# Optimization experiments

Measured on AMD Instinct MI355X. Metric: run time of the kernel, lower is better.

Reference implementation:

```python
import jax, jax.numpy as jnp
import numpy as np

N_NODES = 20000
N_EDGES = 640000
D = 128          # vision_dim == topo_dim
OUT = 256        # out_dim
B = 64           # image batch == num graphs
HW = 64
NEG_SLOPE = 0.2


def _sn(w2d, u):
    """PyTorch spectral_norm forward: one power iteration (u,v detached), W/sigma."""
    v = jax.lax.stop_gradient(w2d.T @ u)
    v = v / (jnp.linalg.norm(v) + 1e-12)
    u2 = jax.lax.stop_gradient(w2d @ v)
    u2 = u2 / (jnp.linalg.norm(u2) + 1e-12)
    sigma = u2 @ (w2d @ v)
    return w2d / sigma


def _leaky(x):
    return jnp.where(x >= 0, x, NEG_SLOPE * x)


def setup_inputs() -> dict:
    key = jax.random.key(0)
    ks = jax.random.split(key, 16)
    vis = jax.random.normal(ks[0], (B, D, HW, HW), dtype=jnp.float32)
    topo = jax.random.normal(ks[1], (N_NODES, D), dtype=jnp.float32)
    edge_index = jax.random.randint(ks[2], (2, N_EDGES), 0, N_NODES, dtype=jnp.int64)
    batch = jnp.sort(jax.random.randint(ks[3], (N_NODES,), 0, B, dtype=jnp.int64))
    s = 0.05
    conv_w = jax.random.normal(ks[4], (D, D, 3, 3), dtype=jnp.float32) * s
    conv_b = jnp.zeros((D,), dtype=jnp.float32)
    conv_u = jax.random.normal(ks[5], (D,), dtype=jnp.float32)
    fcv_w = jax.random.normal(ks[6], (OUT, D * 4), dtype=jnp.float32) * s
    fcv_b = jnp.zeros((OUT,), dtype=jnp.float32)
    fcv_u = jax.random.normal(ks[7], (OUT,), dtype=jnp.float32)
    gcn_w = jax.random.normal(ks[8], (D, D), dtype=jnp.float32) * s
    gcn_b = jnp.zeros((D,), dtype=jnp.float32)
    fct_w = jax.random.normal(ks[9], (OUT, D), dtype=jnp.float32) * s
    fct_b = jnp.zeros((OUT,), dtype=jnp.float32)
    fct_u = jax.random.normal(ks[10], (OUT,), dtype=jnp.float32)
    return dict(vis=vis, topo=topo, edge_index=edge_index, batch=batch,
                conv_w=conv_w, conv_b=conv_b, conv_u=conv_u,
                fcv_w=fcv_w, fcv_b=fcv_b, fcv_u=fcv_u,
                gcn_w=gcn_w, gcn_b=gcn_b,
                fct_w=fct_w, fct_b=fct_b, fct_u=fct_u)


def reference(vis, topo, edge_index, batch,
              conv_w, conv_b, conv_u,
              fcv_w, fcv_b, fcv_u,
              gcn_w, gcn_b,
              fct_w, fct_b, fct_u):
    # ---- vision head: spectral-norm conv3x3 -> leaky_relu -> adaptive max pool 2x2 -> SN linear
    cw = _sn(conv_w.reshape(D, -1), conv_u).reshape(conv_w.shape)
    x = jax.lax.conv_general_dilated(vis, cw, window_strides=(1, 1), padding='VALID',
                                     dimension_numbers=('NCHW', 'OIHW', 'NCHW'))
    x = _leaky(x + conv_b[None, :, None, None])              # [B, D, 62, 62]
    Bc, C, H, W = x.shape
    x = x.reshape(Bc, C, 2, H // 2, 2, W // 2).max(axis=(3, 5))  # adaptive max pool -> [B,D,2,2]
    x = x.reshape(Bc, -1)                                    # [B, 4D]
    vis_score = x @ _sn(fcv_w, fcv_u).T + fcv_b              # [B, OUT]

    # ---- topo head: GCNConv (sym-norm, self-loops) -> leaky_relu -> global max pool -> SN linear
    n = topo.shape[0]
    loop = jnp.arange(n, dtype=edge_index.dtype)
    src = jnp.concatenate([edge_index[0], loop])
    dst = jnp.concatenate([edge_index[1], loop])
    deg = jax.ops.segment_sum(jnp.ones_like(dst, dtype=topo.dtype), dst, num_segments=n)
    dis = jnp.where(deg > 0, jax.lax.rsqrt(jnp.maximum(deg, 1.0)), 0.0)
    norm = dis[src] * dis[dst]                               # [E+N]
    xw = topo @ gcn_w                                        # [N, D]
    h = jax.ops.segment_sum(norm[:, None] * xw[src], dst, num_segments=n) + gcn_b
    h = _leaky(h)
    pooled = jax.ops.segment_max(h, batch, num_segments=B)   # [B, D]
    topo_score = pooled @ _sn(fct_w, fct_u).T + fct_b        # [B, OUT]

    return (vis_score, topo_score)
```

## Files before the change

### kernel.cpp

```cpp
#include <hip/hip_runtime.h>
#include <hip/hip_bf16.h>
#include <float.h>
#include <stdint.h>

#define NB   64
#define CD   128
#define OUTD 256
#define NNODE 20000
#define NEDGE 640000

typedef __bf16 bf16x8 __attribute__((ext_vector_type(8)));
typedef float  f32x4  __attribute__((ext_vector_type(4)));

__device__ inline void gl_lds16(const void* g, void* l) {
  __builtin_amdgcn_global_load_lds(
      (const __attribute__((address_space(1))) void*)g,
      (__attribute__((address_space(3))) void*)l, 16, 0, 0);
}

__device__ inline void atomicMaxF(float* addr, float val) {
  if (val >= 0.f) atomicMax((int*)addr, __float_as_int(val));
  else            atomicMin((unsigned int*)addr, __float_as_uint(val));
}

__global__ void k_init(float* __restrict__ pooled_v, float* __restrict__ pooled_t,
                       int* __restrict__ cnt, int* __restrict__ fill,
                       float* __restrict__ sn_scratch, int* __restrict__ ntotal) {
  const int i = blockIdx.x * 256 + threadIdx.x;
  if (i < NB * CD * 4) pooled_v[i] = -FLT_MAX;
  if (i < NB * CD)     pooled_t[i] = -FLT_MAX;
  if (i < NNODE)       { cnt[i] = 0; fill[i] = 0; }
  if (i < 1796)        sn_scratch[i] = 0.0f;
  if (i == 0)          *ntotal = 0;
}

__global__ __launch_bounds__(256) void k_sn_v(const float* __restrict__ conv_w, const float* __restrict__ conv_u,
                                              const float* __restrict__ fcv_w,  const float* __restrict__ fcv_u,
                                              const float* __restrict__ fct_w,  const float* __restrict__ fct_u,
                                              float* __restrict__ sn) {
  const int bb = blockIdx.x;
  const float* W; const float* u; float* v; int C; int r0;
  if (bb < 4)       { W = conv_w; u = conv_u; v = sn;        C = 1152; r0 = bb * 32; }
  else if (bb < 12) { W = fcv_w;  u = fcv_u;  v = sn + 1152; C = 512;  r0 = (bb - 4) * 32; }
  else              { W = fct_w;  u = fct_u;  v = sn + 1664; C = 128;  r0 = (bb - 12) * 32; }
  const int tid = threadIdx.x;
  float acc[5] = {0.f, 0.f, 0.f, 0.f, 0.f};
  for (int i = r0; i < r0 + 32; ++i) {
    const float ui = u[i];
    const float* row = W + (size_t)i * C;
    #pragma unroll
    for (int t = 0; t < 5; ++t) {
      const int j = tid + t * 256;
      if (j < C) acc[t] += ui * row[j];
    }
  }
  #pragma unroll
  for (int t = 0; t < 5; ++t) {
    const int j = tid + t * 256;
    if (j < C) atomicAdd(&v[j], acc[t]);
  }
}

__global__ __launch_bounds__(256) void k_sn_w(const float* __restrict__ conv_w,
                                              const float* __restrict__ fcv_w,
                                              const float* __restrict__ fct_w,
                                              float* __restrict__ sn) {
  const int gw = blockIdx.x * 4 + (threadIdx.x >> 6);
  const int lane = threadIdx.x & 63;
  const float* W; const float* v; int C, m, row;
  if (gw < 128)      { W = conv_w; v = sn;        C = 1152; m = 0; row = gw; }
  else if (gw < 384) { W = fcv_w;  v = sn + 1152; C = 512;  m = 1; row = gw - 128; }
  else               { W = fct_w;  v = sn + 1664; C = 128;  m = 2; row = gw - 384; }
  const float* wr = W + (size_t)row * C;
  float y = 0.f;
  for (int c = lane; c < C; c += 64) y += wr[c] * v[c];
  #pragma unroll
  for (int s = 32; s > 0; s >>= 1) y += __shfl_xor(y, s, 64);
  if (lane == 0) atomicAdd(&sn[1792 + m], y * y);
}

__global__ __launch_bounds__(256) void k_sn_fin(const float* __restrict__ sn, float* __restrict__ inv_sigma) {
  __shared__ float red[256];
  const int tid = threadIdx.x;
  const int off[4] = {0, 1152, 1664, 1792};
  for (int m = 0; m < 3; ++m) {
    const int C = off[m + 1] - off[m];
    float ss = 0.f;
    for (int j = tid; j < C; j += 256) { const float a = sn[off[m] + j]; ss += a * a; }
    red[tid] = ss; __syncthreads();
    for (int s = 128; s > 0; s >>= 1) { if (tid < s) red[tid] += red[tid + s]; __syncthreads(); }
    if (tid == 0) inv_sigma[m] = (sqrtf(red[0]) + 1e-12f) / sqrtf(sn[1792 + m]);
    __syncthreads();
  }
}

__global__ void k_pack(const float* __restrict__ conv_w, const float* __restrict__ inv_sigma,
                       __hip_bfloat16* __restrict__ Bt2) {
  const int t = blockIdx.x * 256 + threadIdx.x;
  if (t >= 147456) return;
  const int j = t & 7, n = (t >> 3) & 127, s = (t >> 10) & 7, hk = (t >> 13) & 1, tap = t >> 14;
  const int ci = hk * 64 + s * 8 + j;
  Bt2[t] = __float2bfloat16(conv_w[n * 1152 + ci * 9 + tap] * inv_sigma[0]);
}

__global__ __launch_bounds__(256) void k_transpose(const float* __restrict__ vis,
                                                   __hip_bfloat16* __restrict__ visT2) {
  __shared__ float tile[8192];
  const int by = blockIdx.x;
  const int b = by >> 6, y = by & 63;
  const int t = threadIdx.x;
  const float* src = vis + (size_t)b * 524288 + (size_t)(t >> 6) * 4096 + y * 64 + (t & 63);
  #pragma unroll
  for (int i = 0; i < 32; ++i)
    tile[(i * 4 + (t >> 6)) * 64 + (t & 63)] = src[(size_t)i * 4 * 4096];
  __syncthreads();
  bf16x8* dst = (bf16x8*)(visT2 + ((size_t)by << 13));
  #pragma unroll
  for (int k = 0; k < 4; ++k) {
    const int j = k * 256 + t;
    const int g = j >> 6, x = j & 63;
    union { bf16x8 v; __hip_bfloat16 h[8]; } u;
    #pragma unroll
    for (int cc = 0; cc < 8; ++cc)
      u.h[cc] = __float2bfloat16(tile[(g * 8 + cc) * 64 + x]);
    dst[j] = u.v;
  }
}

__global__ __launch_bounds__(256, 4) void k_conv(const __hip_bfloat16* __restrict__ visT2,
                                                 const __hip_bfloat16* __restrict__ Bt2,
                                                 const float* __restrict__ conv_b,
                                                 float* __restrict__ pooled_v) {
  __shared__ bf16x8 lds_a[1024];
  __shared__ bf16x8 lds_b[1024];
  const int bx = blockIdx.x;
  const int b = bx / 31;
  const int y0 = (bx - b * 31) * 2;
  const int tid = threadIdx.x;
  const int wave = tid >> 6, lane = tid & 63;
  const int quad = lane >> 4, l15 = lane & 15;

  f32x4 acc[8][2];
  #pragma unroll
  for (int i = 0; i < 8; ++i) {
    acc[i][0] = f32x4{0.f, 0.f, 0.f, 0.f};
    acc[i][1] = f32x4{0.f, 0.f, 0.f, 0.f};
  }

  const __hip_bfloat16* vb = visT2 + ((size_t)b << 19);
  const int s0 = wave << 1;
  bf16x8* ldsA0 = &lds_a[s0 << 7];
  bf16x8* ldsB0 = &lds_b[s0 << 7];
  const int lane8 = lane << 3;

  for (int ky = 0; ky < 3; ++ky) {
    for (int kx = 0; kx < 3; ++kx) {
      const int tap = ky * 3 + kx;
      #pragma unroll
      for (int hk = 0; hk < 2; ++hk) {
        const __hip_bfloat16* a0p = vb + ((size_t)(((y0 + ky) << 4) + (hk << 3) + s0) << 9) + (kx << 3) + lane8;
        const __hip_bfloat16* a1p = vb + ((size_t)(((y0 + 1 + ky) << 4) + (hk << 3) + s0) << 9) + (kx << 3) + lane8;
        const __hip_bfloat16* bp  = Bt2 + (((size_t)(((tap << 1) + hk) << 3) + s0) << 10) + lane8;
        gl_lds16(a0p,        ldsA0);
        gl_lds16(a1p,        ldsA0 + 64);
        gl_lds16(a0p + 512,  ldsA0 + 128);
        gl_lds16(a1p + 512,  ldsA0 + 192);
        gl_lds16(bp,         ldsB0);
        gl_lds16(bp + 512,   ldsB0 + 64);
        gl_lds16(bp + 1024,  ldsB0 + 128);
        gl_lds16(bp + 1536,  ldsB0 + 192);
        __syncthreads();
        const bf16x8 b00 = lds_b[(quad << 7) + (wave << 5) + l15];
        const bf16x8 b01 = lds_b[(quad << 7) + (wave << 5) + 16 + l15];
        const bf16x8 b10 = lds_b[((4 + quad) << 7) + (wave << 5) + l15];
        const bf16x8 b11 = lds_b[((4 + quad) << 7) + (wave << 5) + 16 + l15];
        #pragma unroll
        for (int mt = 0; mt < 8; ++mt) {
          const bf16x8 a0 = lds_a[(quad << 7) + (mt << 4) + l15];
          const bf16x8 a1 = lds_a[((4 + quad) << 7) + (mt << 4) + l15];
          acc[mt][0] = __builtin_amdgcn_mfma_f32_16x16x32_bf16(a0, b00, acc[mt][0], 0, 0, 0);
          acc[mt][1] = __builtin_amdgcn_mfma_f32_16x16x32_bf16(a0, b01, acc[mt][1], 0, 0, 0);
          acc[mt][0] = __builtin_amdgcn_mfma_f32_16x16x32_bf16(a1, b10, acc[mt][0], 0, 0, 0);
          acc[mt][1] = __builtin_amdgcn_mfma_f32_16x16x32_bf16(a1, b11, acc[mt][1], 0, 0, 0);
        }
        __syncthreads();
      }
    }
  }

  const float cb0 = conv_b[(wave << 5) + l15];
  const float cb1 = conv_b[(wave << 5) + 16 + l15];
  float pmax[2][2][2];
  #pragma unroll
  for (int i = 0; i < 8; ++i) (&pmax[0][0][0])[i] = -FLT_MAX;

  #pragma unroll
  for (int mt = 0; mt < 8; ++mt) {
    const int py = (y0 + (mt >> 2)) >= 31 ? 1 : 0;
    #pragma unroll
    for (int r = 0; r < 4; ++r) {
      const int x = ((mt & 3) << 4) + (quad << 2) + r;
      if (x < 62) {
        const int px = x >= 31 ? 1 : 0;
        float v0 = acc[mt][0][r] + cb0;  v0 = v0 >= 0.f ? v0 : 0.2f * v0;
        float v1 = acc[mt][1][r] + cb1;  v1 = v1 >= 0.f ? v1 : 0.2f * v1;
        pmax[0][py][px] = fmaxf(pmax[0][py][px], v0);
        pmax[1][py][px] = fmaxf(pmax[1][py][px], v1);
      }
    }
  }
  #pragma unroll
  for (int nt = 0; nt < 2; ++nt)
    #pragma unroll
    for (int py = 0; py < 2; ++py)
      #pragma unroll
      for (int px = 0; px < 2; ++px) {
        float v = pmax[nt][py][px];
        v = fmaxf(v, __shfl_xor(v, 16, 64));
        v = fmaxf(v, __shfl_xor(v, 32, 64));
        if (quad == 0) {
          const int n = (wave << 5) + (nt << 4) + l15;
          atomicMaxF(&pooled_v[(size_t)b * 512 + n * 4 + py * 2 + px], v);
        }
      }
}

__global__ __launch_bounds__(256) void k_fcv(const float* __restrict__ pooled_v, const float* __restrict__ fcv_w,
                                             const float* __restrict__ fcv_b, const float* __restrict__ inv_sigma,
                                             float* __restrict__ out) {
  __shared__ f32x4 xr[128];
  const int b = blockIdx.x, tid = threadIdx.x;
  if (tid < 128) xr[tid] = ((const f32x4*)pooled_v)[b * 128 + tid];
  __syncthreads();
  const f32x4* wr = (const f32x4*)(fcv_w + (size_t)tid * 512);
  f32x4 a4 = {0.f, 0.f, 0.f, 0.f};
  for (int f = 0; f < 128; ++f) {
    const f32x4 x = xr[f];
    const f32x4 w = wr[f];
    #pragma unroll
    for (int k = 0; k < 4; ++k) a4[k] += x[k] * w[k];
  }
  const float a = a4[0] + a4[1] + a4[2] + a4[3];
  out[b * 256 + tid] = a * inv_sigma[1] + fcv_b[tid];
}

__global__ void k_deg(const int* __restrict__ dst, int* __restrict__ cnt) {
  const int e = blockIdx.x * 256 + threadIdx.x;
  if (e < NEDGE) atomicAdd(&cnt[dst[e]], 1);
}

__global__ __launch_bounds__(256) void k_scan(const int* __restrict__ cnt, int* __restrict__ offset,
                                              int* __restrict__ total) {
  __shared__ int red[256];
  __shared__ int sbase;
  const int tid = threadIdx.x;
  const int n = blockIdx.x * 256 + tid;
  const int v = (n < NNODE) ? cnt[n] : 0;
  red[tid] = v; __syncthreads();
  for (int d = 1; d < 256; d <<= 1) {
    const int t = (tid >= d) ? red[tid - d] : 0;
    __syncthreads();
    red[tid] += t;
    __syncthreads();
  }
  if (tid == 255) sbase = atomicAdd(total, red[255]);
  __syncthreads();
  if (n < NNODE) offset[n] = sbase + red[tid] - v;
}

__global__ void k_bucket(const int* __restrict__ src, const int* __restrict__ dst,
                         const int* __restrict__ offset, int* __restrict__ fill,
                         int* __restrict__ sorted_src) {
  const int e = blockIdx.x * 256 + threadIdx.x;
  if (e >= NEDGE) return;
  const int t = dst[e];
  const int pos = atomicAdd(&fill[t], 1);
  sorted_src[offset[t] + pos] = src[e];
}

__global__ void k_dis(const int* __restrict__ cnt, float* __restrict__ dis) {
  const int n = blockIdx.x * 256 + threadIdx.x;
  if (n < NNODE) dis[n] = rsqrtf((float)(cnt[n] + 1));
}

__global__ __launch_bounds__(256) void k_xw(const float* __restrict__ topo, const float* __restrict__ gcn_w,
                                            float* __restrict__ xw) {
  __shared__ f32x4 w4[4096];
  const int tid = threadIdx.x;
  const f32x4* gw4 = (const f32x4*)gcn_w;
  for (int i = tid; i < 4096; i += 256) w4[i] = gw4[i];
  __syncthreads();
  const int n0 = blockIdx.x * 64;
  const int jq = tid & 31, ns = tid >> 5;
  for (int pass = 0; pass < 8; ++pass) {
    const int n = n0 + pass * 8 + ns;
    if (n >= NNODE) break;
    const f32x4* tr4 = (const f32x4*)(topo + (size_t)n * 128);
    f32x4 a = {0.f, 0.f, 0.f, 0.f};
    for (int d4 = 0; d4 < 32; ++d4) {
      const f32x4 t = tr4[d4];
      const int base = (d4 << 7) + jq;
      #pragma unroll
      for (int m = 0; m < 4; ++m) {
        const f32x4 w = w4[base + m * 32];
        #pragma unroll
        for (int k = 0; k < 4; ++k) a[k] += t[m] * w[k];
      }
    }
    ((f32x4*)xw)[(size_t)n * 32 + jq] = a;
  }
}

__global__ __launch_bounds__(256) void k_gather(const int* __restrict__ sorted_src,
                                                const int* __restrict__ offset, const int* __restrict__ cnt,
                                                const float* __restrict__ dis, const float* __restrict__ xw,
                                                const float* __restrict__ gcn_b, float* __restrict__ h) {
  __shared__ f32x4 red[256];
  const int n = blockIdx.x;
  const int tid = threadIdx.x;
  const int es = tid >> 5;
  const int d4 = tid & 31;
  const int e0 = offset[n], ne = cnt[n];
  const float dn = dis[n];
  const f32x4* xw4 = (const f32x4*)xw;
  f32x4 a = {0.f, 0.f, 0.f, 0.f};
  if (es == 0) {
    const f32x4 x = xw4[(size_t)n * 32 + d4];
    #pragma unroll
    for (int k = 0; k < 4; ++k) a[k] = dn * x[k];
  }
  for (int e = es; e < ne; e += 8) {
    const int s = sorted_src[e0 + e];
    const float w = dis[s];
    const f32x4 x = xw4[(size_t)s * 32 + d4];
    #pragma unroll
    for (int k = 0; k < 4; ++k) a[k] += w * x[k];
  }
  red[tid] = a;
  __syncthreads();
  if (tid < 128) {
    #pragma unroll
    for (int k = 0; k < 4; ++k) red[tid][k] += red[tid + 128][k];
  }
  __syncthreads();
  if (tid < 64) {
    #pragma unroll
    for (int k = 0; k < 4; ++k) red[tid][k] += red[tid + 64][k];
  }
  __syncthreads();
  if (tid < 32) {
    f32x4 r = red[tid];
    const f32x4 r2 = red[tid + 32];
    const f32x4 gb = ((const f32x4*)gcn_b)[tid];
    f32x4 v;
    #pragma unroll
    for (int k = 0; k < 4; ++k) {
      float t = gb[k] + dn * (r[k] + r2[k]);
      v[k] = t >= 0.f ? t : 0.2f * t;
    }
    ((f32x4*)h)[(size_t)n * 32 + tid] = v;
  }
}

__global__ void k_pool_t(const float* __restrict__ h, const int* __restrict__ batch,
                         float* __restrict__ pooled_t) {
  const int d = threadIdx.x;
  const int n0 = blockIdx.x * 32;
  float run = -FLT_MAX;
  int cur = batch[n0];
  for (int i = 0; i < 32; ++i) {
    const int n = n0 + i;
    const int g = batch[n];
    if (g != cur) {
      atomicMaxF(&pooled_t[cur * 128 + d], run);
      run = -FLT_MAX; cur = g;
    }
    run = fmaxf(run, h[(size_t)n * 128 + d]);
  }
  atomicMaxF(&pooled_t[cur * 128 + d], run);
}

__global__ __launch_bounds__(256) void k_fct(const float* __restrict__ pooled_t, const float* __restrict__ fct_w,
                                             const float* __restrict__ fct_b, const float* __restrict__ inv_sigma,
                                             float* __restrict__ out) {
  __shared__ f32x4 xr[32];
  const int b = blockIdx.x, tid = threadIdx.x;
  if (tid < 32) xr[tid] = ((const f32x4*)pooled_t)[b * 32 + tid];
  __syncthreads();
  const f32x4* wr = (const f32x4*)(fct_w + (size_t)tid * 128);
  f32x4 a4 = {0.f, 0.f, 0.f, 0.f};
  for (int f = 0; f < 32; ++f) {
    const f32x4 x = xr[f];
    const f32x4 w = wr[f];
    #pragma unroll
    for (int k = 0; k < 4; ++k) a4[k] += x[k] * w[k];
  }
  const float a = a4[0] + a4[1] + a4[2] + a4[3];
  out[NB * 256 + b * 256 + tid] = a * inv_sigma[2] + fct_b[tid];
}

extern "C" void kernel_launch(void* const* d_in, const int* in_sizes, int n_in,
                              void* d_out, int out_size, void* d_ws, size_t ws_size,
                              hipStream_t stream) {
  const float* vis    = (const float*)d_in[0];
  const float* topo   = (const float*)d_in[1];
  const int*   eidx   = (const int*)d_in[2];
  const int*   batch  = (const int*)d_in[3];
  const float* conv_w = (const float*)d_in[4];
  const float* conv_b = (const float*)d_in[5];
  const float* conv_u = (const float*)d_in[6];
  const float* fcv_w  = (const float*)d_in[7];
  const float* fcv_b  = (const float*)d_in[8];
  const float* fcv_u  = (const float*)d_in[9];
  const float* gcn_w  = (const float*)d_in[10];
  const float* gcn_b  = (const float*)d_in[11];
  const float* fct_w  = (const float*)d_in[12];
  const float* fct_b  = (const float*)d_in[13];
  const float* fct_u  = (const float*)d_in[14];
  float* out = (float*)d_out;

  char* p = (char*)d_ws;
  float* inv_sigma  = (float*)p; p += 256;
  float* sn_scratch = (float*)p; p += 1796 * 4 + 240;
  float* pooled_v   = (float*)p; p += (size_t)NB * 512 * 4;
  float* pooled_t   = (float*)p; p += (size_t)NB * 128 * 4;
  int*   cnt        = (int*)p;   p += (size_t)NNODE * 4;
  int*   offset     = (int*)p;   p += (size_t)NNODE * 4;
  int*   fill       = (int*)p;   p += (size_t)NNODE * 4;
  float* dis        = (float*)p; p += (size_t)NNODE * 4;
  int*   ntotal     = (int*)p;   p += 256;
  int*   sorted_src = (int*)p;   p += (size_t)NEDGE * 4;
  float* xw         = (float*)p; p += (size_t)NNODE * 128 * 4;
  float* h          = (float*)p; p += (size_t)NNODE * 128 * 4;
  __hip_bfloat16* Bt2 = (__hip_bfloat16*)p; p += (size_t)147456 * 2;
  p = (char*)(((uintptr_t)p + 255) & ~(uintptr_t)255);
  __hip_bfloat16* visT2 = (__hip_bfloat16*)p;

  hipLaunchKernelGGL(k_init,      dim3(128),   dim3(256), 0, stream, pooled_v, pooled_t, cnt, fill, sn_scratch, ntotal);
  hipLaunchKernelGGL(k_sn_v,      dim3(20),    dim3(256), 0, stream, conv_w, conv_u, fcv_w, fcv_u, fct_w, fct_u, sn_scratch);
  hipLaunchKernelGGL(k_sn_w,      dim3(160),   dim3(256), 0, stream, conv_w, fcv_w, fct_w, sn_scratch);
  hipLaunchKernelGGL(k_sn_fin,    dim3(1),     dim3(256), 0, stream, sn_scratch, inv_sigma);
  hipLaunchKernelGGL(k_pack,      dim3(576),   dim3(256), 0, stream, conv_w, inv_sigma, Bt2);
  hipLaunchKernelGGL(k_transpose, dim3(4096),  dim3(256), 0, stream, vis, visT2);
  hipLaunchKernelGGL(k_conv,      dim3(64*31), dim3(256), 0, stream, visT2, Bt2, conv_b, pooled_v);
  hipLaunchKernelGGL(k_fcv,       dim3(64),    dim3(256), 0, stream, pooled_v, fcv_w, fcv_b, inv_sigma, out);
  hipLaunchKernelGGL(k_deg,       dim3(2500),  dim3(256), 0, stream, eidx + NEDGE, cnt);
  hipLaunchKernelGGL(k_scan,      dim3(79),    dim3(256), 0, stream, cnt, offset, ntotal);
  hipLaunchKernelGGL(k_bucket,    dim3(2500),  dim3(256), 0, stream, eidx, eidx + NEDGE, offset, fill, sorted_src);
  hipLaunchKernelGGL(k_dis,       dim3(79),    dim3(256), 0, stream, cnt, dis);
  hipLaunchKernelGGL(k_xw,        dim3(313),   dim3(256), 0, stream, topo, gcn_w, xw);
  hipLaunchKernelGGL(k_gather,    dim3(NNODE), dim3(256), 0, stream, sorted_src, offset, cnt, dis, xw, gcn_b, h);
  hipLaunchKernelGGL(k_pool_t,    dim3(625),   dim3(128), 0, stream, h, batch, pooled_t);
  hipLaunchKernelGGL(k_fct,       dim3(64),    dim3(256), 0, stream, pooled_t, fct_w, fct_b, inv_sigma, out);
}
```

Measured before the change: 588.2 us.

## Store prescaled xw and h in bf16, wave-per-node gather, fuse small kernels

```diff
diff --git a/kernel.cpp b/kernel.cpp
--- a/kernel.cpp
+++ b/kernel.cpp
@@ -10,6 +10,7 @@
 #define NEDGE 640000
 
 typedef __bf16 bf16x8 __attribute__((ext_vector_type(8)));
+typedef __bf16 bf16x4 __attribute__((ext_vector_type(4)));
 typedef float  f32x4  __attribute__((ext_vector_type(4)));
 
 __device__ inline void gl_lds16(const void* g, void* l) {
@@ -225,32 +226,13 @@
       }
 }
 
-__global__ __launch_bounds__(256) void k_fcv(const float* __restrict__ pooled_v, const float* __restrict__ fcv_w,
-                                             const float* __restrict__ fcv_b, const float* __restrict__ inv_sigma,
-                                             float* __restrict__ out) {
-  __shared__ f32x4 xr[128];
-  const int b = blockIdx.x, tid = threadIdx.x;
-  if (tid < 128) xr[tid] = ((const f32x4*)pooled_v)[b * 128 + tid];
-  __syncthreads();
-  const f32x4* wr = (const f32x4*)(fcv_w + (size_t)tid * 512);
-  f32x4 a4 = {0.f, 0.f, 0.f, 0.f};
-  for (int f = 0; f < 128; ++f) {
-    const f32x4 x = xr[f];
-    const f32x4 w = wr[f];
-    #pragma unroll
-    for (int k = 0; k < 4; ++k) a4[k] += x[k] * w[k];
-  }
-  const float a = a4[0] + a4[1] + a4[2] + a4[3];
-  out[b * 256 + tid] = a * inv_sigma[1] + fcv_b[tid];
-}
-
 __global__ void k_deg(const int* __restrict__ dst, int* __restrict__ cnt) {
   const int e = blockIdx.x * 256 + threadIdx.x;
   if (e < NEDGE) atomicAdd(&cnt[dst[e]], 1);
 }
 
 __global__ __launch_bounds__(256) void k_scan(const int* __restrict__ cnt, int* __restrict__ offset,
-                                              int* __restrict__ total) {
+                                              int* __restrict__ total, float* __restrict__ dis) {
   __shared__ int red[256];
   __shared__ int sbase;
   const int tid = threadIdx.x;
@@ -265,7 +247,10 @@
   }
   if (tid == 255) sbase = atomicAdd(total, red[255]);
   __syncthreads();
-  if (n < NNODE) offset[n] = sbase + red[tid] - v;
+  if (n < NNODE) {
+    offset[n] = sbase + red[tid] - v;
+    dis[n] = rsqrtf((float)(v + 1));
+  }
 }
 
 __global__ void k_bucket(const int* __restrict__ src, const int* __restrict__ dst,
@@ -278,13 +263,8 @@
   sorted_src[offset[t] + pos] = src[e];
 }
 
-__global__ void k_dis(const int* __restrict__ cnt, float* __restrict__ dis) {
-  const int n = blockIdx.x * 256 + threadIdx.x;
-  if (n < NNODE) dis[n] = rsqrtf((float)(cnt[n] + 1));
-}
-
 __global__ __launch_bounds__(256) void k_xw(const float* __restrict__ topo, const float* __restrict__ gcn_w,
-                                            float* __restrict__ xw) {
+                                            const float* __restrict__ dis, __bf16* __restrict__ xws) {
   __shared__ f32x4 w4[4096];
   const int tid = threadIdx.x;
   const f32x4* gw4 = (const f32x4*)gcn_w;
@@ -307,62 +287,57 @@
         for (int k = 0; k < 4; ++k) a[k] += t[m] * w[k];
       }
     }
-    ((f32x4*)xw)[(size_t)n * 32 + jq] = a;
+    const float dn = dis[n];
+    bf16x4 o;
+    #pragma unroll
+    for (int k = 0; k < 4; ++k) o[k] = (__bf16)(a[k] * dn);
+    ((bf16x4*)xws)[(size_t)n * 32 + jq] = o;
   }
 }
 
 __global__ __launch_bounds__(256) void k_gather(const int* __restrict__ sorted_src,
                                                 const int* __restrict__ offset, const int* __restrict__ cnt,
-                                                const float* __restrict__ dis, const float* __restrict__ xw,
-                                                const float* __restrict__ gcn_b, float* __restrict__ h) {
-  __shared__ f32x4 red[256];
-  const int n = blockIdx.x;
-  const int tid = threadIdx.x;
-  const int es = tid >> 5;
-  const int d4 = tid & 31;
+                                                const float* __restrict__ dis, const __bf16* __restrict__ xws,
+                                                const float* __restrict__ gcn_b, __bf16* __restrict__ h) {
+  const int wave = threadIdx.x >> 6, lane = threadIdx.x & 63;
+  const int n = blockIdx.x * 4 + wave;
+  const int slot = lane >> 4, l16 = lane & 15;
   const int e0 = offset[n], ne = cnt[n];
-  const float dn = dis[n];
-  const f32x4* xw4 = (const f32x4*)xw;
-  f32x4 a = {0.f, 0.f, 0.f, 0.f};
-  if (es == 0) {
-    const f32x4 x = xw4[(size_t)n * 32 + d4];
-    #pragma unroll
-    for (int k = 0; k < 4; ++k) a[k] = dn * x[k];
-  }
-  for (int e = es; e < ne; e += 8) {
+  const bf16x8* x8 = (const bf16x8*)xws;
+  float a[8];
+  if (slot == 0) {
+    const bf16x8 v = x8[(size_t)n * 16 + l16];
+    #pragma unroll
+    for (int k = 0; k < 8; ++k) a[k] = (float)v[k];
+  } else {
+    #pragma unroll
+    for (int k = 0; k < 8; ++k) a[k] = 0.f;
+  }
+  for (int e = slot; e < ne; e += 4) {
     const int s = sorted_src[e0 + e];
-    const float w = dis[s];
-    const f32x4 x = xw4[(size_t)s * 32 + d4];
-    #pragma unroll
-    for (int k = 0; k < 4; ++k) a[k] += w * x[k];
-  }
-  red[tid] = a;
-  __syncthreads();
-  if (tid < 128) {
-    #pragma unroll
-    for (int k = 0; k < 4; ++k) red[tid][k] += red[tid + 128][k];
-  }
-  __syncthreads();
-  if (tid < 64) {
-    #pragma unroll
-    for (int k = 0; k < 4; ++k) red[tid][k] += red[tid + 64][k];
-  }
-  __syncthreads();
-  if (tid < 32) {
-    f32x4 r = red[tid];
-    const f32x4 r2 = red[tid + 32];
-    const f32x4 gb = ((const f32x4*)gcn_b)[tid];
-    f32x4 v;
-    #pragma unroll
-    for (int k = 0; k < 4; ++k) {
-      float t = gb[k] + dn * (r[k] + r2[k]);
-      v[k] = t >= 0.f ? t : 0.2f * t;
-    }
-    ((f32x4*)h)[(size_t)n * 32 + tid] = v;
-  }
-}
-
-__global__ void k_pool_t(const float* __restrict__ h, const int* __restrict__ batch,
+    const bf16x8 v = x8[(size_t)s * 16 + l16];
+    #pragma unroll
+    for (int k = 0; k < 8; ++k) a[k] += (float)v[k];
+  }
+  #pragma unroll
+  for (int k = 0; k < 8; ++k) {
+    a[k] += __shfl_xor(a[k], 16, 64);
+    a[k] += __shfl_xor(a[k], 32, 64);
+  }
+  if (slot == 0) {
+    const float dn = dis[n];
+    bf16x8 o;
+    #pragma unroll
+    for (int k = 0; k < 8; ++k) {
+      float t = gcn_b[(l16 << 3) + k] + dn * a[k];
+      t = t >= 0.f ? t : 0.2f * t;
+      o[k] = (__bf16)t;
+    }
+    ((bf16x8*)h)[(size_t)n * 16 + l16] = o;
+  }
+}
+
+__global__ void k_pool_t(const __bf16* __restrict__ h, const int* __restrict__ batch,
                          float* __restrict__ pooled_t) {
   const int d = threadIdx.x;
   const int n0 = blockIdx.x * 32;
@@ -375,28 +350,48 @@
       atomicMaxF(&pooled_t[cur * 128 + d], run);
       run = -FLT_MAX; cur = g;
     }
-    run = fmaxf(run, h[(size_t)n * 128 + d]);
+    run = fmaxf(run, (float)h[(size_t)n * 128 + d]);
   }
   atomicMaxF(&pooled_t[cur * 128 + d], run);
 }
 
-__global__ __launch_bounds__(256) void k_fct(const float* __restrict__ pooled_t, const float* __restrict__ fct_w,
-                                             const float* __restrict__ fct_b, const float* __restrict__ inv_sigma,
-                                             float* __restrict__ out) {
-  __shared__ f32x4 xr[32];
-  const int b = blockIdx.x, tid = threadIdx.x;
-  if (tid < 32) xr[tid] = ((const f32x4*)pooled_t)[b * 32 + tid];
-  __syncthreads();
-  const f32x4* wr = (const f32x4*)(fct_w + (size_t)tid * 128);
-  f32x4 a4 = {0.f, 0.f, 0.f, 0.f};
-  for (int f = 0; f < 32; ++f) {
-    const f32x4 x = xr[f];
-    const f32x4 w = wr[f];
-    #pragma unroll
-    for (int k = 0; k < 4; ++k) a4[k] += x[k] * w[k];
-  }
-  const float a = a4[0] + a4[1] + a4[2] + a4[3];
-  out[NB * 256 + b * 256 + tid] = a * inv_sigma[2] + fct_b[tid];
+__global__ __launch_bounds__(256) void k_fc(const float* __restrict__ pooled_v, const float* __restrict__ fcv_w,
+                                            const float* __restrict__ fcv_b,
+                                            const float* __restrict__ pooled_t, const float* __restrict__ fct_w,
+                                            const float* __restrict__ fct_b,
+                                            const float* __restrict__ inv_sigma, float* __restrict__ out) {
+  const int tid = threadIdx.x;
+  if (blockIdx.x < 64) {
+    __shared__ f32x4 xr[128];
+    const int b = blockIdx.x;
+    if (tid < 128) xr[tid] = ((const f32x4*)pooled_v)[b * 128 + tid];
+    __syncthreads();
+    const f32x4* wr = (const f32x4*)(fcv_w + (size_t)tid * 512);
+    f32x4 a4 = {0.f, 0.f, 0.f, 0.f};
+    for (int f = 0; f < 128; ++f) {
+      const f32x4 x = xr[f];
+      const f32x4 w = wr[f];
+      #pragma unroll
+      for (int k = 0; k < 4; ++k) a4[k] += x[k] * w[k];
+    }
+    const float a = a4[0] + a4[1] + a4[2] + a4[3];
+    out[b * 256 + tid] = a * inv_sigma[1] + fcv_b[tid];
+  } else {
+    __shared__ f32x4 xr2[32];
+    const int b = blockIdx.x - 64;
+    if (tid < 32) xr2[tid] = ((const f32x4*)pooled_t)[b * 32 + tid];
+    __syncthreads();
+    const f32x4* wr = (const f32x4*)(fct_w + (size_t)tid * 128);
+    f32x4 a4 = {0.f, 0.f, 0.f, 0.f};
+    for (int f = 0; f < 32; ++f) {
+      const f32x4 x = xr2[f];
+      const f32x4 w = wr[f];
+      #pragma unroll
+      for (int k = 0; k < 4; ++k) a4[k] += x[k] * w[k];
+    }
+    const float a = a4[0] + a4[1] + a4[2] + a4[3];
+    out[NB * 256 + b * 256 + tid] = a * inv_sigma[2] + fct_b[tid];
+  }
 }
 
 extern "C" void kernel_launch(void* const* d_in, const int* in_sizes, int n_in,
@@ -430,8 +425,8 @@
   float* dis        = (float*)p; p += (size_t)NNODE * 4;
   int*   ntotal     = (int*)p;   p += 256;
   int*   sorted_src = (int*)p;   p += (size_t)NEDGE * 4;
-  float* xw         = (float*)p; p += (size_t)NNODE * 128 * 4;
-  float* h          = (float*)p; p += (size_t)NNODE * 128 * 4;
+  __bf16* xws       = (__bf16*)p; p += (size_t)NNODE * 128 * 2 + 256;
+  __bf16* h         = (__bf16*)p; p += (size_t)NNODE * 128 * 2 + 256;
   __hip_bfloat16* Bt2 = (__hip_bfloat16*)p; p += (size_t)147456 * 2;
   p = (char*)(((uintptr_t)p + 255) & ~(uintptr_t)255);
   __hip_bfloat16* visT2 = (__hip_bfloat16*)p;
@@ -443,13 +438,11 @@
   hipLaunchKernelGGL(k_pack,      dim3(576),   dim3(256), 0, stream, conv_w, inv_sigma, Bt2);
   hipLaunchKernelGGL(k_transpose, dim3(4096),  dim3(256), 0, stream, vis, visT2);
   hipLaunchKernelGGL(k_conv,      dim3(64*31), dim3(256), 0, stream, visT2, Bt2, conv_b, pooled_v);
-  hipLaunchKernelGGL(k_fcv,       dim3(64),    dim3(256), 0, stream, pooled_v, fcv_w, fcv_b, inv_sigma, out);
   hipLaunchKernelGGL(k_deg,       dim3(2500),  dim3(256), 0, stream, eidx + NEDGE, cnt);
-  hipLaunchKernelGGL(k_scan,      dim3(79),    dim3(256), 0, stream, cnt, offset, ntotal);
+  hipLaunchKernelGGL(k_scan,      dim3(79),    dim3(256), 0, stream, cnt, offset, ntotal, dis);
   hipLaunchKernelGGL(k_bucket,    dim3(2500),  dim3(256), 0, stream, eidx, eidx + NEDGE, offset, fill, sorted_src);
-  hipLaunchKernelGGL(k_dis,       dim3(79),    dim3(256), 0, stream, cnt, dis);
-  hipLaunchKernelGGL(k_xw,        dim3(313),   dim3(256), 0, stream, topo, gcn_w, xw);
-  hipLaunchKernelGGL(k_gather,    dim3(NNODE), dim3(256), 0, stream, sorted_src, offset, cnt, dis, xw, gcn_b, h);
+  hipLaunchKernelGGL(k_xw,        dim3(313),   dim3(256), 0, stream, topo, gcn_w, dis, xws);
+  hipLaunchKernelGGL(k_gather,    dim3(5000),  dim3(256), 0, stream, sorted_src, offset, cnt, dis, xws, gcn_b, h);
   hipLaunchKernelGGL(k_pool_t,    dim3(625),   dim3(128), 0, stream, h, batch, pooled_t);
-  hipLaunchKernelGGL(k_fct,       dim3(64),    dim3(256), 0, stream, pooled_t, fct_w, fct_b, inv_sigma, out);
-}
+  hipLaunchKernelGGL(k_fc,        dim3(128),   dim3(256), 0, stream, pooled_v, fcv_w, fcv_b, pooled_t, fct_w, fct_b, inv_sigma, out);
+}
```

Result: faster. 554.6 us (-5.7%).
